# Performance work log

Hardware: AMD Instinct MI355X
Metric: run time of the kernel (lower is better)

## Reference

```python
import jax, jax.numpy as jnp
import numpy as np

H = 50  # hidden size (hardcoded in the torch module)

def lstm_cell(h, c, xt, Wih, Whh, bih, bhh):
    # xt: [B, D]; gates packed PyTorch-style: i, f, g, o each of size H
    gates = xt @ Wih.T + h @ Whh.T + bih + bhh  # [B, 4H]
    i, f, g, o = jnp.split(gates, 4, axis=-1)
    i = jax.nn.sigmoid(i)
    f = jax.nn.sigmoid(f)
    g = jnp.tanh(g)
    o = jax.nn.sigmoid(o)
    c_new = f * c + i * g
    h_new = o * jnp.tanh(c_new)
    return h_new, c_new

def lstm_last_hidden(x, Wih, Whh, bih, bhh):
    # x: [B, T, D] -> final hidden state h_T: [B, H] (zero init state)
    B = x.shape[0]
    h0 = jnp.zeros((B, H), dtype=x.dtype)
    c0 = jnp.zeros((B, H), dtype=x.dtype)
    def step(carry, xt):
        h, c = carry
        h, c = lstm_cell(h, c, xt, Wih, Whh, bih, bhh)
        return (h, c), None
    (hT, _), _ = jax.lax.scan(step, (h0, c0), jnp.swapaxes(x, 0, 1))
    return hT

def setup_inputs() -> dict:
    key = jax.random.key(0)
    ks = jax.random.split(key, 11)
    s = 1.0 / np.sqrt(H)  # PyTorch LSTM/Linear init scale
    u = lambda k, shape: jax.random.uniform(k, shape, jnp.float32, -s, s)
    return {
        'x': jax.random.normal(ks[0], (2048, 1024, 1), jnp.float32),
        'lstm1_Wih': u(ks[1], (4 * H, 1)),
        'lstm1_Whh': u(ks[2], (4 * H, H)),
        'lstm1_bih': u(ks[3], (4 * H,)),
        'lstm1_bhh': u(ks[4], (4 * H,)),
        'lstm2_Wih': u(ks[5], (4 * H, H)),
        'lstm2_Whh': u(ks[6], (4 * H, H)),
        'lstm2_bih': u(ks[7], (4 * H,)),
        'lstm2_bhh': u(ks[8], (4 * H,)),
        'fc_W': u(ks[9], (1, H)),
        'fc_b': u(ks[10], (1,)),
    }

def reference(x, lstm1_Wih, lstm1_Whh, lstm1_bih, lstm1_bhh,
              lstm2_Wih, lstm2_Whh, lstm2_bih, lstm2_bhh, fc_W, fc_b):
    # lstm1 over full sequence; only the last timestep output is used downstream
    h1 = lstm_last_hidden(x, lstm1_Wih, lstm1_Whh, lstm1_bih, lstm1_bhh)  # [B, H]
    # lstm2 sees a length-1 sequence starting from zero state -> one cell step
    B = x.shape[0]
    z = jnp.zeros((B, H), dtype=x.dtype)
    h2, _ = lstm_cell(z, z, h1, lstm2_Wih, lstm2_Whh, lstm2_bih, lstm2_bhh)  # [B, H]
    return h2 @ fc_W.T + fc_b  # [B, 1]
```

## Files before the change

kernel.cpp:

```cpp
#include <hip/hip_runtime.h>

#define HH 50
#define TT 1024
#define BT 8
#define NB (2048 / BT)
#define CHUNK 256
#define XST 260
#define HST 72

typedef _Float16 half8 __attribute__((ext_vector_type(8)));
typedef float f32x4 __attribute__((ext_vector_type(4)));

union H8 { half8 v; _Float16 h[8]; unsigned short u[8]; unsigned int i[4]; };

__device__ __forceinline__ float rcp_f(float x) { return __builtin_amdgcn_rcpf(x); }

#if __has_builtin(__builtin_amdgcn_exp2f)
__device__ __forceinline__ float exp2_f(float x) { return __builtin_amdgcn_exp2f(x); }
#else
__device__ __forceinline__ float exp2_f(float x) { return __expf(0.6931471805599453f * x); }
#endif

#define L2E   1.4426950408889634f
#define L2E2  2.8853900817779268f

__device__ __forceinline__ float sigm_n(float a) {
    return rcp_f(1.0f + exp2_f(a));
}
__device__ __forceinline__ float tanh_p(float a) {
    return __builtin_fmaf(-2.0f, rcp_f(1.0f + exp2_f(a)), 1.0f);
}
__device__ __forceinline__ unsigned short f2h(float f) {
    return __builtin_bit_cast(unsigned short, (_Float16)f);
}
__device__ __forceinline__ float bperm(int addr, float v) {
    return __builtin_bit_cast(float,
        __builtin_amdgcn_ds_bpermute(addr, __builtin_bit_cast(int, v)));
}

__global__ __launch_bounds__(256) void lstm_mfma_kernel(
    const float* __restrict__ x,
    const float* __restrict__ wih1, const float* __restrict__ whh1,
    const float* __restrict__ bih1, const float* __restrict__ bhh1,
    const float* __restrict__ wih2,
    const float* __restrict__ bih2, const float* __restrict__ bhh2,
    const float* __restrict__ fcw,  const float* __restrict__ fcb,
    float* __restrict__ out)
{
    __shared__ float xs[BT * XST];
    __shared__ __align__(16) unsigned short hb[2][16 * HST];
    __shared__ float h2s[BT * 52];

    const int tid  = threadIdx.x;
    const int wv   = tid >> 6;
    const int js   = wv;
    const int lane = tid & 63;
    const int l16  = lane & 15;
    const int quad = lane >> 4;
    const int j    = js * 16 + l16;
    const bool jv  = (j < HH);
    const bool q2  = (quad == 2);
    const int b0   = blockIdx.x * BT;
    const int  srcl  = (((quad & 1) << 4) + l16) * 4;
    const bool qlow  = (quad < 2);
    const int  bm0   = ((quad & 1) << 2) + ((quad >> 1) << 1);

    H8 bw[4][2];
    #pragma unroll
    for (int t4 = 0; t4 < 4; ++t4) {
        const float sc = (t4 == 2) ? L2E2 : -L2E;
        const int row = t4 * HH + j;
        #pragma unroll
        for (int kk = 0; kk < 2; ++kk)
            #pragma unroll
            for (int e = 0; e < 8; ++e) {
                const int k = kk * 32 + quad * 8 + e;
                const float v = (jv && k < HH) ? whh1[row * HH + k] * sc : 0.0f;
                bw[t4][kk].h[e] = (_Float16)v;
            }
        if (q2) {
            const float bsc = jv ? (bih1[row] + bhh1[row]) * sc : 0.0f;
            const _Float16 bhi = (_Float16)bsc;
            bw[t4][1].h[2] = (_Float16)(jv ? wih1[row] * sc : 0.0f);
            bw[t4][1].h[3] = bhi;
            bw[t4][1].h[4] = (_Float16)(bsc - (float)bhi);
        }
    }

    for (int i = tid; i < 2 * 16 * HST; i += 256) {
        const int col = i % HST;
        ((unsigned short*)hb)[i] = (col == 51 || col == 52) ? 0x3c00 : 0;
    }

    float c0 = 0.f, c1 = 0.f;
    const f32x4 kZ = {0.f, 0.f, 0.f, 0.f};
    const bool xw = (wv == 0) && (lane < BT);

    auto cell = [&](float ai, float af, float ag, float ao, float& cc) -> unsigned short {
        const float Ei = exp2_f(ai), Ef = exp2_f(af), Eg = exp2_f(ag), Eo = exp2_f(ao);
        const float pf  = 1.0f + Ef;
        const float P   = (1.0f + Ei) * (1.0f + Eg);
        const float den = pf * P;
        const float num = __builtin_fmaf(cc, P, (Eg - 1.0f) * pf);
        cc = num * rcp_f(den);
        const float ac = fminf(cc * L2E2, 80.0f);
        const float Ec = exp2_f(ac);
        const float h  = (Ec - 1.0f) * rcp_f((1.0f + Eo) * (1.0f + Ec));
        return f2h(h);
    };

#define REDIST(G, P0, P1)                                                              \
    {                                                                                  \
        const float r1 = bperm(srcl, acc[G][2]);                                       \
        const float r2 = bperm(srcl, acc[G][3]);                                       \
        P0 = qlow ? acc[G][0] : r1;                                                    \
        P1 = qlow ? acc[G][1] : r2;                                                    \
    }

#define STEP(T, CUR, NXT, STAGEOK)                                                     \
    {                                                                                  \
        const int tc = (T) & (CHUNK - 1);                                              \
        if (STAGEOK && tc == 0) {                                                      \
            for (int i = tid; i < BT * (CHUNK / 4); i += 256) {                        \
                const int r = i >> 6, c4 = i & 63;                                     \
                const float4 q = ((const float4*)x)[((b0 + r) * TT + (T)) / 4 + c4];   \
                *(float4*)&xs[r * XST + c4 * 4] = q;                                   \
            }                                                                          \
            __syncthreads();                    \
        }                                                                              \
        H8 a0, a1;                                                                     \
        a0.v = *(const half8*)&(CUR)[l16 * HST + quad * 8];                            \
        a1.v = *(const half8*)&(CUR)[l16 * HST + 32 + quad * 8];                       \
        if (STAGEOK && tc == 0) {                                                      \
             \
            const float xv = (l16 < BT) ? xs[l16 * XST] : 0.0f;                        \
            const unsigned int pk = 0x3c000000u | (unsigned int)f2h(xv);               \
            a1.i[1] = q2 ? pk : a1.i[1];                                               \
            a1.i[2] = q2 ? 0x00003c00u : a1.i[2];                                      \
        }                                                                              \
        float xnext = 0.0f;                                                            \
        if (xw) xnext = xs[lane * XST + ((tc + 1) & (CHUNK - 1))];                     \
        f32x4 acc[4];                                                                  \
        _Pragma("unroll")                                                              \
        for (int t4 = 0; t4 < 4; ++t4) {                                               \
            acc[t4] = __builtin_amdgcn_mfma_f32_16x16x32_f16(a0.v, bw[t4][0].v, kZ, 0, 0, 0);       \
            acc[t4] = __builtin_amdgcn_mfma_f32_16x16x32_f16(a1.v, bw[t4][1].v, acc[t4], 0, 0, 0);  \
        }                                                                              \
        float pi0, pi1, pf0, pf1, pg0, pg1, po0, po1;                                  \
        REDIST(0, pi0, pi1) REDIST(1, pf0, pf1)                                        \
        REDIST(2, pg0, pg1) REDIST(3, po0, po1)                                        \
        const unsigned short h0 = cell(pi0, pf0, pg0, po0, c0);                        \
        const unsigned short h1 = cell(pi1, pf1, pg1, po1, c1);                        \
        if (jv) {                \
            (NXT)[bm0 * HST + j]       = h0;                                           \
            (NXT)[(bm0 + 1) * HST + j] = h1;                                           \
        }                                                                              \
        if (xw) (NXT)[lane * HST + 50] = f2h(xnext);  \
        __syncthreads();                                                               \
    }

    for (int t = 0; t < TT; t += 2) {
        STEP(t,     hb[0], hb[1], true);
        STEP(t + 1, hb[1], hb[0], false);
    }
#undef STEP
#undef REDIST
    unsigned short* cur = hb[0];

    {
        H8 bw2[4][2];
        float b2[4];
        #pragma unroll
        for (int t4 = 0; t4 < 4; ++t4) {
            const float sc = (t4 == 2) ? L2E2 : -L2E;
            const int row = t4 * HH + j;
            #pragma unroll
            for (int kk = 0; kk < 2; ++kk)
                #pragma unroll
                for (int e = 0; e < 8; ++e) {
                    const int k = kk * 32 + quad * 8 + e;
                    const float v = (jv && k < HH) ? wih2[row * HH + k] * sc : 0.0f;
                    bw2[t4][kk].h[e] = (_Float16)v;
                }
            b2[t4] = jv ? (bih2[row] + bhh2[row]) * sc : 0.0f;
        }
        H8 a0, a1;
        a0.v = *(const half8*)&cur[l16 * HST + quad * 8];
        a1.v = *(const half8*)&cur[l16 * HST + 32 + quad * 8];
        f32x4 acc2[4];
        #pragma unroll
        for (int t4 = 0; t4 < 4; ++t4) {
            const f32x4 cb = {b2[t4], b2[t4], b2[t4], b2[t4]};
            acc2[t4] = __builtin_amdgcn_mfma_f32_16x16x32_f16(a0.v, bw2[t4][0].v, cb, 0, 0, 0);
            acc2[t4] = __builtin_amdgcn_mfma_f32_16x16x32_f16(a1.v, bw2[t4][1].v, acc2[t4], 0, 0, 0);
        }
        #pragma unroll
        for (int r = 0; r < 4; ++r) {
            const int b = quad * 4 + r;
            const float ig = sigm_n(acc2[0][r]);
            const float gg = tanh_p(acc2[2][r]);
            const float og = sigm_n(acc2[3][r]);
            const float cc = ig * gg;
            const float h2 = og * tanh_p(cc * L2E2);
            if (b < BT && jv) h2s[b * 52 + j] = h2;
        }
    }
    __syncthreads();

    if (tid < BT * 16) {
        const int b = tid >> 4, l = tid & 15;
        float p = 0.f;
        for (int jj = l; jj < HH; jj += 16)
            p = __builtin_fmaf(h2s[b * 52 + jj], fcw[jj], p);
        #pragma unroll
        for (int off = 8; off > 0; off >>= 1) p += __shfl_xor(p, off, 16);
        if (l == 0) out[b0 + b] = p + fcb[0];
    }
}

extern "C" void kernel_launch(void* const* d_in, const int* in_sizes, int n_in,
                              void* d_out, int out_size, void* d_ws, size_t ws_size,
                              hipStream_t stream) {
    lstm_mfma_kernel<<<NB, 256, 0, stream>>>(
        (const float*)d_in[0],
        (const float*)d_in[1], (const float*)d_in[2],
        (const float*)d_in[3], (const float*)d_in[4],
        (const float*)d_in[5],
        (const float*)d_in[7], (const float*)d_in[8],
        (const float*)d_in[9], (const float*)d_in[10],
        (float*)d_out);
}
```

Baseline: 507.7 us.

## Halve batch per block, stage full x upfront, use permlane swaps for gate redistribution

Shrinks the batch tile per block from 8 to 4 rows so each lane computes one cell instead of two, doubling the number of blocks. The whole input sequence for the block is now loaded into LDS once before the loop, which removes the per-chunk staging branch and its extra barrier. The cross-lane gate redistribution moves from ds_bpermute to v_permlane16/32_swap instructions so the LDS crossbar is not used. In exchange, half of each MFMA tile's rows do no useful work, total MFMA work doubles, and LDS use per block grows.

After: 520.4 us. 1.03x slower.

```diff
diff --git a/kernel.cpp b/kernel.cpp
--- a/kernel.cpp
+++ b/kernel.cpp
@@ -2,10 +2,9 @@
 
 #define HH 50
 #define TT 1024
-#define BT 8
+#define BT 4
 #define NB (2048 / BT)
-#define CHUNK 256
-#define XST 260
+#define XSTF 1028
 #define HST 72
 
 typedef _Float16 half8 __attribute__((ext_vector_type(8)));
@@ -32,10 +31,6 @@
 }
 __device__ __forceinline__ unsigned short f2h(float f) {
     return __builtin_bit_cast(unsigned short, (_Float16)f);
-}
-__device__ __forceinline__ float bperm(int addr, float v) {
-    return __builtin_bit_cast(float,
-        __builtin_amdgcn_ds_bpermute(addr, __builtin_bit_cast(int, v)));
 }
 
 __global__ __launch_bounds__(256) void lstm_mfma_kernel(
@@ -47,7 +42,7 @@
     const float* __restrict__ fcw,  const float* __restrict__ fcb,
     float* __restrict__ out)
 {
-    __shared__ float xs[BT * XST];
+    __shared__ float xs[BT * XSTF];
     __shared__ __align__(16) unsigned short hb[2][16 * HST];
     __shared__ float h2s[BT * 52];
 
@@ -61,9 +56,6 @@
     const bool jv  = (j < HH);
     const bool q2  = (quad == 2);
     const int b0   = blockIdx.x * BT;
-    const int  srcl  = (((quad & 1) << 4) + l16) * 4;
-    const bool qlow  = (quad < 2);
-    const int  bm0   = ((quad & 1) << 2) + ((quad >> 1) << 1);
 
     H8 bw[4][2];
     #pragma unroll
@@ -92,9 +84,20 @@
         ((unsigned short*)hb)[i] = (col == 51 || col == 52) ? 0x3c00 : 0;
     }
 
-    float c0 = 0.f, c1 = 0.f;
+    for (int i = tid; i < BT * (TT / 4); i += 256) {
+        const int r = i >> 8, c4 = i & 255;
+        const float4 q = ((const float4*)x)[((b0 + r) * TT) / 4 + c4];
+        *(float4*)&xs[r * XSTF + c4 * 4] = q;
+    }
+    if (tid < BT * 4) xs[(tid >> 2) * XSTF + 1024 + (tid & 3)] = 0.0f;
+    __syncthreads();
+
+    const bool xw = (wv == 0) && (lane < BT);
+    if (xw) hb[0][lane * HST + 50] = f2h(xs[lane * XSTF]);
+    __syncthreads();
+
+    float c = 0.f;
     const f32x4 kZ = {0.f, 0.f, 0.f, 0.f};
-    const bool xw = (wv == 0) && (lane < BT);
 
     auto cell = [&](float ai, float af, float ag, float ao, float& cc) -> unsigned short {
         const float Ei = exp2_f(ai), Ef = exp2_f(af), Eg = exp2_f(ag), Eo = exp2_f(ao);
@@ -109,59 +112,40 @@
         return f2h(h);
     };
 
-#define REDIST(G, P0, P1)                                                              \
-    {                                                                                  \
-        const float r1 = bperm(srcl, acc[G][2]);                                       \
-        const float r2 = bperm(srcl, acc[G][3]);                                       \
-        P0 = qlow ? acc[G][0] : r1;                                                    \
-        P1 = qlow ? acc[G][1] : r2;                                                    \
-    }
-
-#define STEP(T, CUR, NXT, STAGEOK)                                                     \
-    {                                                                                  \
-        const int tc = (T) & (CHUNK - 1);                                              \
-        if (STAGEOK && tc == 0) {                                                      \
-            for (int i = tid; i < BT * (CHUNK / 4); i += 256) {                        \
-                const int r = i >> 6, c4 = i & 63;                                     \
-                const float4 q = ((const float4*)x)[((b0 + r) * TT + (T)) / 4 + c4];   \
-                *(float4*)&xs[r * XST + c4 * 4] = q;                                   \
-            }                                                                          \
-            __syncthreads();                    \
-        }                                                                              \
-        H8 a0, a1;                                                                     \
-        a0.v = *(const half8*)&(CUR)[l16 * HST + quad * 8];                            \
-        a1.v = *(const half8*)&(CUR)[l16 * HST + 32 + quad * 8];                       \
-        if (STAGEOK && tc == 0) {                                                      \
-             \
-            const float xv = (l16 < BT) ? xs[l16 * XST] : 0.0f;                        \
-            const unsigned int pk = 0x3c000000u | (unsigned int)f2h(xv);               \
-            a1.i[1] = q2 ? pk : a1.i[1];                                               \
-            a1.i[2] = q2 ? 0x00003c00u : a1.i[2];                                      \
-        }                                                                              \
-        float xnext = 0.0f;                                                            \
-        if (xw) xnext = xs[lane * XST + ((tc + 1) & (CHUNK - 1))];                     \
-        f32x4 acc[4];                                                                  \
-        _Pragma("unroll")                                                              \
-        for (int t4 = 0; t4 < 4; ++t4) {                                               \
+#define REDIST(G, PG)                                                          \
+    {                                                                          \
+        float xx0 = acc[G][0], xx1 = acc[G][1];                                \
+        float yy0 = acc[G][2], yy1 = acc[G][3];                                \
+        asm("v_permlane16_swap_b32 %0, %1" : "+v"(xx0), "+v"(xx1));            \
+        asm("v_permlane16_swap_b32 %0, %1" : "+v"(yy0), "+v"(yy1));            \
+        asm("v_permlane32_swap_b32 %0, %1" : "+v"(xx0), "+v"(yy0));            \
+        PG = xx0;                                                              \
+    }
+
+#define STEP(T, CUR, NXT)                                                      \
+    {                                                                          \
+        H8 a0, a1;                                                             \
+        a0.v = *(const half8*)&(CUR)[l16 * HST + quad * 8];                    \
+        a1.v = *(const half8*)&(CUR)[l16 * HST + 32 + quad * 8];               \
+        float xnext = 0.0f;                                                    \
+        if (xw) xnext = xs[lane * XSTF + (T) + 1];                             \
+        f32x4 acc[4];                                                          \
+        _Pragma("unroll")                                                      \
+        for (int t4 = 0; t4 < 4; ++t4) {                                       \
             acc[t4] = __builtin_amdgcn_mfma_f32_16x16x32_f16(a0.v, bw[t4][0].v, kZ, 0, 0, 0);       \
             acc[t4] = __builtin_amdgcn_mfma_f32_16x16x32_f16(a1.v, bw[t4][1].v, acc[t4], 0, 0, 0);  \
-        }                                                                              \
-        float pi0, pi1, pf0, pf1, pg0, pg1, po0, po1;                                  \
-        REDIST(0, pi0, pi1) REDIST(1, pf0, pf1)                                        \
-        REDIST(2, pg0, pg1) REDIST(3, po0, po1)                                        \
-        const unsigned short h0 = cell(pi0, pf0, pg0, po0, c0);                        \
-        const unsigned short h1 = cell(pi1, pf1, pg1, po1, c1);                        \
-        if (jv) {                \
-            (NXT)[bm0 * HST + j]       = h0;                                           \
-            (NXT)[(bm0 + 1) * HST + j] = h1;                                           \
-        }                                                                              \
-        if (xw) (NXT)[lane * HST + 50] = f2h(xnext);  \
-        __syncthreads();                                                               \
+        }                                                                      \
+        float p0, p1, p2, p3;                                                  \
+        REDIST(0, p0) REDIST(1, p1) REDIST(2, p2) REDIST(3, p3)                \
+        const unsigned short hv = cell(p0, p1, p2, p3, c);                     \
+        if (jv) (NXT)[quad * HST + j] = hv;   \
+        if (xw) (NXT)[lane * HST + 50] = f2h(xnext);                           \
+        __syncthreads();                                                       \
     }
 
     for (int t = 0; t < TT; t += 2) {
-        STEP(t,     hb[0], hb[1], true);
-        STEP(t + 1, hb[1], hb[0], false);
+        STEP(t,     hb[0], hb[1]);
+        STEP(t + 1, hb[1], hb[0]);
     }
 #undef STEP
 #undef REDIST
```
